# Optimization experiments

Measured on AMD Instinct MI355X. Metric: run time of the kernel, lower is better.

Reference implementation:

```python
import jax, jax.numpy as jnp
import numpy as np

GRID_SIZE = 4
ORDER = 3
NUM_BASIS = GRID_SIZE + ORDER  # 7
KNOTS = jnp.linspace(-1.0, 1.0, NUM_BASIS + ORDER + 1)  # 11 knots


def _normalise(x):
    # eval-mode with uninitialized running stats: use batch min/max
    min_val = x.min(axis=0)
    max_val = x.max(axis=0)
    width = jnp.maximum(max_val - min_val, 0.01)
    centre = 0.5 * (max_val + min_val)
    scaled = (x - centre) / (0.5 * width)
    return jnp.clip(scaled, -2.0, 2.0)


def _bspline_basis(x):
    # x: (B, I) -> basis: (B, I, NUM_BASIS), de Boor recursion vectorized over i
    xe = x[..., None]  # (B, I, 1)
    idx = jnp.arange(NUM_BASIS)
    left, right = KNOTS[idx], KNOTS[idx + 1]
    basis = ((xe >= left) & (xe < right)).astype(x.dtype)
    last = jnp.where(xe[..., 0] == KNOTS[NUM_BASIS], 1.0, basis[..., -1])
    basis = basis.at[..., -1].set(last)
    for k in range(1, ORDER + 1):
        d1 = KNOTS[idx + k] - KNOTS[idx]
        d2 = KNOTS[idx + k + 1] - KNOTS[idx + 1]
        b_next = jnp.concatenate([basis[..., 1:], jnp.zeros_like(basis[..., :1])], axis=-1)
        t1 = jnp.where(d1 > 0, (xe - KNOTS[idx]) / jnp.where(d1 > 0, d1, 1.0), 0.0) * basis
        t2 = jnp.where(d2 > 0, (KNOTS[idx + k + 1] - xe) / jnp.where(d2 > 0, d2, 1.0), 0.0) * b_next
        basis = t1 + t2
    return basis


def setup_inputs() -> dict:
    key = jax.random.key(0)
    k1, k2, k3 = jax.random.split(key, 3)
    B, I, O = 8192, 256, 256
    x = jax.random.normal(k1, (B, I), dtype=jnp.float32)
    # xavier-uniform base_weight
    bound = float(np.sqrt(6.0 / (I + O)))
    base_weight = jax.random.uniform(k2, (O, I), minval=-bound, maxval=bound, dtype=jnp.float32)
    spline_weight = jnp.ones((O, I), dtype=jnp.float32)
    spline_coeff = 0.001 * jax.random.normal(k3, (O, I, NUM_BASIS), dtype=jnp.float32)
    bias = jnp.zeros((O,), dtype=jnp.float32)
    return {"x": x, "base_weight": base_weight, "spline_weight": spline_weight,
            "spline_coeff": spline_coeff, "bias": bias}


def reference(x, base_weight, spline_weight, spline_coeff, bias):
    x_norm = _normalise(x)                          # (B, I)
    basis = _bspline_basis(x_norm)                  # (B, I, M)
    silu_x = x_norm * jax.nn.sigmoid(x_norm)        # (B, I)
    base_out = silu_x @ base_weight.T               # sum_i silu_i * W_oi -> (B, O)
    coeff_scaled = spline_coeff * spline_weight[..., None]  # (O, I, M)
    spline_out = jnp.einsum('bim,oim->bo', basis, coeff_scaled)
    return base_out + spline_out + bias[None, :]
```

## Files before the change

### kernel.cpp

```cpp
#include <hip/hip_runtime.h>
#include <hip/hip_bf16.h>
#include <stdint.h>

#define B_SZ 8192
#define I_SZ 256
#define O_SZ 256
#define KDIM 2048
#define BMB 128
#define BNB 64
#define FT 16
#define NTILE 16
#define NPART 128

typedef __bf16 bf16x8 __attribute__((ext_vector_type(8)));
typedef float f32x4 __attribute__((ext_vector_type(4)));

__global__ __launch_bounds__(256) void minmax_partial(
    const float* __restrict__ x, float* __restrict__ pmin,
    float* __restrict__ pmax) {
  const int cg = threadIdx.x & 63;
  const int rs = threadIdx.x >> 6;
  const int r0 = blockIdx.x * 64;
  const float* p = x + (size_t)(r0 + rs) * I_SZ + cg * 4;
  float4 mn = {1e30f, 1e30f, 1e30f, 1e30f};
  float4 mx = {-1e30f, -1e30f, -1e30f, -1e30f};
#pragma unroll
  for (int k = 0; k < 16; ++k) {
    const float4 v = *reinterpret_cast<const float4*>(p + (size_t)k * 4 * I_SZ);
    mn.x = fminf(mn.x, v.x); mn.y = fminf(mn.y, v.y);
    mn.z = fminf(mn.z, v.z); mn.w = fminf(mn.w, v.w);
    mx.x = fmaxf(mx.x, v.x); mx.y = fmaxf(mx.y, v.y);
    mx.z = fmaxf(mx.z, v.z); mx.w = fmaxf(mx.w, v.w);
  }
  __shared__ float rmn[4][I_SZ], rmx[4][I_SZ];
  *reinterpret_cast<float4*>(&rmn[rs][cg * 4]) = mn;
  *reinterpret_cast<float4*>(&rmx[rs][cg * 4]) = mx;
  __syncthreads();
  if (threadIdx.x < 64) {
    float4 a, b;
    const int c0 = threadIdx.x * 4;
    a.x = fminf(fminf(rmn[0][c0+0], rmn[1][c0+0]), fminf(rmn[2][c0+0], rmn[3][c0+0]));
    a.y = fminf(fminf(rmn[0][c0+1], rmn[1][c0+1]), fminf(rmn[2][c0+1], rmn[3][c0+1]));
    a.z = fminf(fminf(rmn[0][c0+2], rmn[1][c0+2]), fminf(rmn[2][c0+2], rmn[3][c0+2]));
    a.w = fminf(fminf(rmn[0][c0+3], rmn[1][c0+3]), fminf(rmn[2][c0+3], rmn[3][c0+3]));
    b.x = fmaxf(fmaxf(rmx[0][c0+0], rmx[1][c0+0]), fmaxf(rmx[2][c0+0], rmx[3][c0+0]));
    b.y = fmaxf(fmaxf(rmx[0][c0+1], rmx[1][c0+1]), fmaxf(rmx[2][c0+1], rmx[3][c0+1]));
    b.z = fmaxf(fmaxf(rmx[0][c0+2], rmx[1][c0+2]), fmaxf(rmx[2][c0+2], rmx[3][c0+2]));
    b.w = fmaxf(fmaxf(rmx[0][c0+3], rmx[1][c0+3]), fmaxf(rmx[2][c0+3], rmx[3][c0+3]));
    *reinterpret_cast<float4*>(&pmin[blockIdx.x * I_SZ + c0]) = a;
    *reinterpret_cast<float4*>(&pmax[blockIdx.x * I_SZ + c0]) = b;
  }
}

__global__ void pack_W(const float* __restrict__ bw,
                       const float* __restrict__ sw,
                       const float* __restrict__ coeff,
                       __hip_bfloat16* __restrict__ W,
                       const float* __restrict__ pmin,
                       const float* __restrict__ pmax,
                       float* __restrict__ cenrhw) {
  const int idx = blockIdx.x * blockDim.x + threadIdx.x;
  const int i = idx & (I_SZ - 1);
  const int o = idx >> 8;
  const float s = sw[idx];
  union { __hip_bfloat16 h[8]; float4 f4; } u;
#pragma unroll
  for (int m = 0; m < 7; ++m)
    u.h[m] = __float2bfloat16(coeff[(size_t)idx * 7 + m] * s);
  u.h[7] = __float2bfloat16(bw[idx]);
  const size_t off = (size_t)o * KDIM + (size_t)((i ^ (o & 7)) << 3);
  *reinterpret_cast<float4*>(&W[off]) = u.f4;

  if (blockIdx.x == 0) {
    const int c = threadIdx.x;
    float mn = 1e30f, mx = -1e30f;
#pragma unroll 8
    for (int p = 0; p < NPART; ++p) {
      mn = fminf(mn, pmin[p * I_SZ + c]);
      mx = fmaxf(mx, pmax[p * I_SZ + c]);
    }
    const float width = fmaxf(mx - mn, 0.01f);
    const float rhw = 2.0f / width;
    cenrhw[2 * c]     = rhw;
    cenrhw[2 * c + 1] = -0.5f * (mx + mn) * rhw;
  }
}

__device__ __forceinline__ void async16(const __hip_bfloat16* g, __hip_bfloat16* l) {
  __builtin_amdgcn_global_load_lds(
      (const __attribute__((address_space(1))) void*)g,
      (__attribute__((address_space(3))) void*)l, 16, 0, 0);
}

__device__ __forceinline__ uint32_t bfc(float f) {
  union { __hip_bfloat16 b; unsigned short s; } c;
  c.b = __float2bfloat16(f);
  return (uint32_t)c.s;
}

__device__ __forceinline__ bf16x8 evalOne(float xv, float2 s2) {
  const float xn = __builtin_fmaf(xv, s2.x, s2.y);
  const float sp = __builtin_fmaf(xn, 5.0f, 5.0f);
  const float c6 = fminf(fmaxf(floorf(sp), 0.0f), 6.0f);
  const int ci = (int)c6;
  const float u = sp - c6;
  const float zm = (sp > 7.0f) ? 0.0f : (1.0f / 6.0f);
  const float u2 = u * u, u3 = u2 * u, t1 = 1.0f - u;
  const float q3 = u3 * zm;
  const float q0 = (t1 * t1) * (t1 * zm);
  float h2 = __builtin_fmaf(-3.0f, u, 3.0f);
  h2 = __builtin_fmaf(h2, u, 3.0f);
  h2 = __builtin_fmaf(h2, u, 1.0f);
  float h1 = __builtin_fmaf(3.0f, u, -6.0f);
  h1 = __builtin_fmaf(h1, u2, 4.0f);
  const float q2v = h2 * zm, q1v = h1 * zm;
  const float silu = xn * __builtin_amdgcn_rcpf(1.0f + __expf(-xn));
  const uint64_t D = (uint64_t)(bfc(q0) | (bfc(q1v) << 16)) |
                     ((uint64_t)(bfc(q2v) | (bfc(q3) << 16)) << 32);
  const int tt = ci * 16 - 48;
  const uint64_t ls = D << (tt & 63);
  const uint64_t rs = D >> ((-tt) & 63);
  uint64_t lo = (tt >= 0) ? ls : rs;
  uint64_t hi = (tt >= 0) ? ((D >> ((63 - tt) & 63)) >> 1) : 0ull;
  hi = (hi & 0x0000FFFFFFFFFFFFull) | ((uint64_t)bfc(silu) << 48);
  union { uint32_t w[4]; bf16x8 v; } r;
  r.w[0] = (uint32_t)lo; r.w[1] = (uint32_t)(lo >> 32);
  r.w[2] = (uint32_t)hi; r.w[3] = (uint32_t)(hi >> 32);
  return r.v;
}

__global__ __launch_bounds__(256) void gemm_fused(
    const float* __restrict__ x, const __hip_bfloat16* __restrict__ W,
    const float* __restrict__ cenrhw, const float* __restrict__ bias,
    float* __restrict__ out) {
  __shared__ __align__(16) __hip_bfloat16 Blds[2][BNB * FT * 8];
  __shared__ float2 scl[I_SZ];

  const int t = threadIdx.x;
  const int lane = t & 63;
  const int wave = t >> 6;
  const int fr = lane & 15, fk = lane >> 4;

  const int bid = blockIdx.x;
  const int swz = (bid & 7) * 32 + (bid >> 3);
  const int bm = swz >> 2, bn = swz & 3;
  const int r0 = bm * BMB, c0 = bn * BNB;

  scl[t] = reinterpret_cast<const float2*>(cenrhw)[t];

  const __hip_bfloat16* gb = W + (size_t)(c0 + (t >> 4)) * KDIM + (t & 15) * 8;

  auto stageB = [&](int buf, int kt) {
    const __hip_bfloat16* g = gb + kt * 128;
#pragma unroll
    for (int q = 0; q < 4; ++q)
      async16(g + (size_t)16 * q * KDIM, &Blds[buf][(t + 256 * q) * 8]);
  };

  const float* xq = x + (size_t)(r0 + wave * 32 + fr) * I_SZ + fk;

  f32x4 acc[2][4] = {{{0,0,0,0},{0,0,0,0},{0,0,0,0},{0,0,0,0}},
                     {{0,0,0,0},{0,0,0,0},{0,0,0,0},{0,0,0,0}}};

  stageB(0, 0);
  float xv0[4], xv1[4], xn0[4], xn1[4];
#pragma unroll
  for (int s = 0; s < 4; ++s) {
    xv0[s] = xq[4 * s];
    xv1[s] = xq[16 * I_SZ + 4 * s];
  }
  __syncthreads();

  for (int kt = 0; kt < NTILE; ++kt) {
    const int buf = kt & 1;
    if (kt + 1 < NTILE) {
      stageB(buf ^ 1, kt + 1);
      const int o = (kt + 1) * 16;
#pragma unroll
      for (int s = 0; s < 4; ++s) {
        xn0[s] = xq[o + 4 * s];
        xn1[s] = xq[16 * I_SZ + o + 4 * s];
      }
    }
    bf16x8 af0[4], af1[4];
#pragma unroll
    for (int s = 0; s < 4; ++s) {
      const float2 s2 = scl[kt * 16 + 4 * s + fk];
      af0[s] = evalOne(xv0[s], s2);
      af1[s] = evalOne(xv1[s], s2);
    }
    const __hip_bfloat16* L = Blds[buf];
#pragma unroll
    for (int s = 0; s < 4; ++s) {
      bf16x8 bg[4];
#pragma unroll
      for (int n = 0; n < 4; ++n) {
        const int row = n * 16 + fr;
        const int unit = (4 * s + fk) ^ (row & 7);
        bg[n] = *reinterpret_cast<const bf16x8*>(&L[row * 128 + unit * 8]);
      }
#pragma unroll
      for (int n = 0; n < 4; ++n) {
        acc[0][n] = __builtin_amdgcn_mfma_f32_16x16x32_bf16(af0[s], bg[n], acc[0][n], 0, 0, 0);
        acc[1][n] = __builtin_amdgcn_mfma_f32_16x16x32_bf16(af1[s], bg[n], acc[1][n], 0, 0, 0);
      }
    }
    if (kt + 1 < NTILE) {
      asm volatile("s_waitcnt vmcnt(8)" ::: "memory");
      __builtin_amdgcn_s_barrier();
#pragma unroll
      for (int s = 0; s < 4; ++s) { xv0[s] = xn0[s]; xv1[s] = xn1[s]; }
    }
  }

#pragma unroll
  for (int m = 0; m < 2; ++m)
#pragma unroll
    for (int n = 0; n < 4; ++n) {
      const int col = c0 + n * 16 + fr;
      const float bc = bias[col];
#pragma unroll
      for (int r = 0; r < 4; ++r) {
        const int row = r0 + wave * 32 + m * 16 + fk * 4 + r;
        out[(size_t)row * O_SZ + col] = acc[m][n][r] + bc;
      }
    }
}

extern "C" void kernel_launch(void* const* d_in, const int* in_sizes, int n_in,
                              void* d_out, int out_size, void* d_ws, size_t ws_size,
                              hipStream_t stream) {
  const float* x     = (const float*)d_in[0];
  const float* bw    = (const float*)d_in[1];
  const float* sw    = (const float*)d_in[2];
  const float* coeff = (const float*)d_in[3];
  const float* bias  = (const float*)d_in[4];
  float* out = (float*)d_out;

  char* ws = (char*)d_ws;
  __hip_bfloat16* Wbuf = (__hip_bfloat16*)ws;
  float* pmin   = (float*)(ws + (size_t)O_SZ * KDIM * 2);
  float* pmax   = pmin + NPART * I_SZ;
  float* cenrhw = pmax + NPART * I_SZ;

  minmax_partial<<<NPART, 256, 0, stream>>>(x, pmin, pmax);
  pack_W<<<(O_SZ * I_SZ) / 256, 256, 0, stream>>>(bw, sw, coeff, Wbuf,
                                                  pmin, pmax, cenrhw);
  gemm_fused<<<(B_SZ / BMB) * (O_SZ / BNB), 256, 0, stream>>>(x, Wbuf, cenrhw,
                                                              bias, out);
}
```

Baseline: 48.86 us.

## Stage half of weight K-range into LDS at once instead of double-buffered tiles

Replaces the per-16-feature double-buffered B tile pipeline with two large stages, each loading a 64x1024 bf16 half of the weight panel into LDS. This removes fifteen per-tile barriers and waitcnts, leaving one pair of barriers between the halves. In exchange the first load is large and fully exposed with no overlap against compute. LDS use grows to about 128KB, which will likely cut occupancy to one block per CU.

```diff
diff --git a/kernel.cpp b/kernel.cpp
--- a/kernel.cpp
+++ b/kernel.cpp
@@ -8,8 +8,6 @@
 #define KDIM 2048
 #define BMB 128
 #define BNB 64
-#define FT 16
-#define NTILE 16
 #define NPART 128
 
 typedef __bf16 bf16x8 __attribute__((ext_vector_type(8)));
@@ -133,7 +131,7 @@
     const float* __restrict__ x, const __hip_bfloat16* __restrict__ W,
     const float* __restrict__ cenrhw, const float* __restrict__ bias,
     float* __restrict__ out) {
-  __shared__ __align__(16) __hip_bfloat16 Blds[2][BNB * FT * 8];
+  __shared__ __align__(16) __hip_bfloat16 Wlds[BNB][1024];
   __shared__ float2 scl[I_SZ];
 
   const int t = threadIdx.x;
@@ -148,13 +146,13 @@
 
   scl[t] = reinterpret_cast<const float2*>(cenrhw)[t];
 
-  const __hip_bfloat16* gb = W + (size_t)(c0 + (t >> 4)) * KDIM + (t & 15) * 8;
-
-  auto stageB = [&](int buf, int kt) {
-    const __hip_bfloat16* g = gb + kt * 128;
-#pragma unroll
-    for (int q = 0; q < 4; ++q)
-      async16(g + (size_t)16 * q * KDIM, &Blds[buf][(t + 256 * q) * 8]);
+  const __hip_bfloat16* gw = W + (size_t)(c0 + (t >> 7)) * KDIM + (t & 127) * 8;
+  auto stageW = [&](int h) {
+    const __hip_bfloat16* g = gw + h * 1024;
+    __hip_bfloat16* l = &Wlds[0][0] + (size_t)t * 8;
+#pragma unroll
+    for (int q = 0; q < 32; ++q)
+      async16(g + (size_t)2 * q * KDIM, l + (size_t)2048 * q);
   };
 
   const float* xq = x + (size_t)(r0 + wave * 32 + fr) * I_SZ + fk;
@@ -162,54 +160,57 @@
   f32x4 acc[2][4] = {{{0,0,0,0},{0,0,0,0},{0,0,0,0},{0,0,0,0}},
                      {{0,0,0,0},{0,0,0,0},{0,0,0,0},{0,0,0,0}}};
 
-  stageB(0, 0);
-  float xv0[4], xv1[4], xn0[4], xn1[4];
-#pragma unroll
-  for (int s = 0; s < 4; ++s) {
-    xv0[s] = xq[4 * s];
-    xv1[s] = xq[16 * I_SZ + 4 * s];
+  stageW(0);
+  float xc0[4], xc1[4], xn0[4], xn1[4];
+#pragma unroll
+  for (int s2 = 0; s2 < 4; ++s2) {
+    xc0[s2] = xq[4 * s2];
+    xc1[s2] = xq[16 * I_SZ + 4 * s2];
   }
   __syncthreads();
 
-  for (int kt = 0; kt < NTILE; ++kt) {
-    const int buf = kt & 1;
-    if (kt + 1 < NTILE) {
-      stageB(buf ^ 1, kt + 1);
-      const int o = (kt + 1) * 16;
-#pragma unroll
-      for (int s = 0; s < 4; ++s) {
-        xn0[s] = xq[o + 4 * s];
-        xn1[s] = xq[16 * I_SZ + o + 4 * s];
+#pragma unroll 1
+  for (int h = 0; h < 2; ++h) {
+#pragma unroll 1
+    for (int g = 0; g < 8; ++g) {
+      const int gn = h * 8 + g + 1;
+      if (gn < 16) {
+        const int off = gn * 16;
+#pragma unroll
+        for (int s2 = 0; s2 < 4; ++s2) {
+          xn0[s2] = xq[off + 4 * s2];
+          xn1[s2] = xq[16 * I_SZ + off + 4 * s2];
+        }
       }
-    }
-    bf16x8 af0[4], af1[4];
-#pragma unroll
-    for (int s = 0; s < 4; ++s) {
-      const float2 s2 = scl[kt * 16 + 4 * s + fk];
-      af0[s] = evalOne(xv0[s], s2);
-      af1[s] = evalOne(xv1[s], s2);
-    }
-    const __hip_bfloat16* L = Blds[buf];
-#pragma unroll
-    for (int s = 0; s < 4; ++s) {
-      bf16x8 bg[4];
-#pragma unroll
-      for (int n = 0; n < 4; ++n) {
-        const int row = n * 16 + fr;
-        const int unit = (4 * s + fk) ^ (row & 7);
-        bg[n] = *reinterpret_cast<const bf16x8*>(&L[row * 128 + unit * 8]);
+#pragma unroll
+      for (int s2 = 0; s2 < 4; ++s2) {
+        const int gs = g * 4 + s2;
+        const int f = h * 128 + gs * 4 + fk;
+        const float2 s2c = scl[f];
+        const bf16x8 a0 = evalOne(xc0[s2], s2c);
+        const bf16x8 a1 = evalOne(xc1[s2], s2c);
+        const int cp = gs * 4 + fk;
+        const int grp = cp & ~7, low = cp & 7;
+        bf16x8 bg[4];
+#pragma unroll
+        for (int n = 0; n < 4; ++n) {
+          const int row = n * 16 + fr;
+          const int cidx = grp | (low ^ (row & 7));
+          bg[n] = *reinterpret_cast<const bf16x8*>(&Wlds[row][cidx * 8]);
+        }
+#pragma unroll
+        for (int n = 0; n < 4; ++n) {
+          acc[0][n] = __builtin_amdgcn_mfma_f32_16x16x32_bf16(a0, bg[n], acc[0][n], 0, 0, 0);
+          acc[1][n] = __builtin_amdgcn_mfma_f32_16x16x32_bf16(a1, bg[n], acc[1][n], 0, 0, 0);
+        }
       }
 #pragma unroll
-      for (int n = 0; n < 4; ++n) {
-        acc[0][n] = __builtin_amdgcn_mfma_f32_16x16x32_bf16(af0[s], bg[n], acc[0][n], 0, 0, 0);
-        acc[1][n] = __builtin_amdgcn_mfma_f32_16x16x32_bf16(af1[s], bg[n], acc[1][n], 0, 0, 0);
-      }
-    }
-    if (kt + 1 < NTILE) {
-      asm volatile("s_waitcnt vmcnt(8)" ::: "memory");
-      __builtin_amdgcn_s_barrier();
-#pragma unroll
-      for (int s = 0; s < 4; ++s) { xv0[s] = xn0[s]; xv1[s] = xn1[s]; }
+      for (int s2 = 0; s2 < 4; ++s2) { xc0[s2] = xn0[s2]; xc1[s2] = xn1[s2]; }
+    }
+    if (h == 0) {
+      __syncthreads();
+      stageW(1);
+      __syncthreads();
     }
   }
 
```

Measured after the change: 44.52 us. -8.9%, faster.
